# Performance work log

Measured on AMD Instinct MI355X. Metric: run time of the kernel, lower is better.

## Reference

```python
import jax, jax.numpy as jnp
import numpy as np

B, T, D, H, O = 128, 512, 128, 256, 1


def setup_inputs() -> dict:
    key = jax.random.key(0)
    ks = jax.random.split(key, 11)
    s = lambda n: 1.0 / np.sqrt(H)
    u = lambda k, shape: jax.random.uniform(k, shape, jnp.float32, -s(0), s(0))
    return {
        "X": jax.random.normal(ks[0], (B, T, D), jnp.float32),
        "Wih0": u(ks[1], (4 * H, D)),
        "Whh0": u(ks[2], (4 * H, H)),
        "bih0": u(ks[3], (4 * H,)),
        "bhh0": u(ks[4], (4 * H,)),
        "Wih1": u(ks[5], (4 * H, H)),
        "Whh1": u(ks[6], (4 * H, H)),
        "bih1": u(ks[7], (4 * H,)),
        "bhh1": u(ks[8], (4 * H,)),
        "Wfc": u(ks[9], (O, H)),
        "bfc": u(ks[10], (O,)),
    }


def _lstm_layer(x, Wih, Whh, bih, bhh):
    # x: [B, T, Din] -> h sequence [B, T, H]
    # Precompute input contributions for all timesteps (one big GEMM).
    xg = jnp.einsum("btd,gd->btg", x, Wih) + bih + bhh  # [B, T, 4H]
    xg = jnp.transpose(xg, (1, 0, 2))  # [T, B, 4H]
    h0 = jnp.zeros((x.shape[0], Whh.shape[1]), x.dtype)
    c0 = jnp.zeros_like(h0)

    def step(carry, xt):
        h, c = carry
        gates = xt + h @ Whh.T  # [B, 4H]
        i, f, g, o = jnp.split(gates, 4, axis=-1)  # PyTorch gate order i,f,g,o
        i = jax.nn.sigmoid(i)
        f = jax.nn.sigmoid(f)
        g = jnp.tanh(g)
        o = jax.nn.sigmoid(o)
        c = f * c + i * g
        h = o * jnp.tanh(c)
        return (h, c), h

    (_, _), hs = jax.lax.scan(step, (h0, c0), xg)
    return jnp.transpose(hs, (1, 0, 2))  # [B, T, H]


def reference(X, Wih0, Whh0, bih0, bhh0, Wih1, Whh1, bih1, bhh1, Wfc, bfc):
    h1 = _lstm_layer(X, Wih0, Whh0, bih0, bhh0)
    h2 = _lstm_layer(h1, Wih1, Whh1, bih1, bhh1)
    return h2[:, -1, :] @ Wfc.T + bfc  # [B, O]
```

## Files before the change

kernel.cpp:

```cpp
#include <hip/hip_runtime.h>

typedef unsigned short u16;
typedef unsigned int u32;
typedef __attribute__((ext_vector_type(8))) short bf8;
typedef __attribute__((ext_vector_type(4))) float f4;

#define DEVI static __device__ __forceinline__

constexpr int Bb = 128, Tt = 512, Dd = 128, Hh = 256, G4 = 1024;
constexpr int CH  = 32;
constexpr int NCH = Tt / CH;
constexpr int MCH = CH * Bb;
constexpr size_t CHF = (size_t)MCH * G4;

DEVI u16 f2bf(float f) {
  union { float f; u32 u; } v; v.f = f;
  u32 r = v.u + 0x7FFFu + ((v.u >> 16) & 1u);
  return (u16)(r >> 16);
}
DEVI float bf2f(u16 b) { union { u32 u; float f; } v; v.u = ((u32)b) << 16; return v.f; }
DEVI float frcp(float x) { return __builtin_amdgcn_rcpf(x); }
DEVI float sigm(float x) { return frcp(1.f + __expf(-x)); }
DEVI float tanh_f(float x) { return 1.f - 2.f * frcp(1.f + __expf(2.f * x)); }
DEVI f4 mfma16(bf8 a, bf8 b, f4 c) {
  return __builtin_amdgcn_mfma_f32_16x16x32_bf16(a, b, c, 0, 0, 0);
}

DEVI u32 ld_u32_coh(const u32* p) {
  u32 r;
  asm volatile("global_load_dword %0, %1, off sc0 sc1\ns_waitcnt vmcnt(0)"
               : "=&v"(r) : "v"(p) : "memory");
  return r;
}
DEVI bf8 ld16_coh(const u16* p) {
  bf8 r;
  asm volatile("global_load_dwordx4 %0, %1, off sc0 sc1" : "=&v"(r) : "v"(p) : "memory");
  return r;
}
DEVI void st16_coh(u16* p, bf8 v) {
  asm volatile("global_store_dwordx4 %0, %1, off sc0 sc1" :: "v"(p), "v"(v) : "memory");
}
DEVI void st_u32_coh(u32* p, u32 v) {
  asm volatile("global_store_dword %0, %1, off sc0 sc1" :: "v"(p), "v"(v) : "memory");
}
DEVI f4 ld16f(const float* p) {
  f4 r;
  asm volatile("global_load_dwordx4 %0, %1, off" : "=&v"(r) : "v"(p) : "memory");
  return r;
}


__global__ void k_prep_x(const float* __restrict__ X, u16* __restrict__ Xhi, u16* __restrict__ Xlo) {
  size_t idx = (size_t)blockIdx.x * 256 + threadIdx.x;
  int d = (int)(idx % Dd);
  size_t bt = idx / Dd;
  int b = (int)(bt / Tt), t = (int)(bt % Tt);
  float x = X[idx];
  u16 hi = f2bf(x);
  u16 lo = f2bf(x - bf2f(hi));
  size_t o = ((size_t)t * Bb + b) * Dd + d;
  Xhi[o] = hi; Xlo[o] = lo;
}

__global__ void k_split(const float* __restrict__ W, u16* __restrict__ hi_, u16* __restrict__ lo_) {
  size_t idx = (size_t)blockIdx.x * 256 + threadIdx.x;
  float v = W[idx];
  u16 hi = f2bf(v);
  hi_[idx] = hi;
  lo_[idx] = f2bf(v - bf2f(hi));
}

__global__ void k_prep_whh(const float* __restrict__ Whh, u16* __restrict__ W2) {
  int idx = blockIdx.x * 256 + threadIdx.x;
  int i = idx & 7, lane = (idx >> 3) & 63, kt = (idx >> 9) & 7, jtg = idx >> 12;
  int jp = (jtg << 4) + (lane & 15);
  int k  = ((lane >> 4) << 3) + i + (kt << 5);
  W2[idx] = f2bf(Whh[(size_t)jp * Hh + k]);
}

__global__ void k_bias(const float* __restrict__ a, const float* __restrict__ b, float* __restrict__ o) {
  int i = blockIdx.x * 256 + threadIdx.x;
  if (i < G4) o[i] = a[i] + b[i];
}

__global__ void k_init(u32* __restrict__ tags) {
  int i = blockIdx.x * 256 + threadIdx.x;
  if (i < 2 * (Tt + 1) * 64) {
    int row = (i >> 6) % (Tt + 1);
    tags[i] = (row == 0) ? 1u : 0u;
  }
}

__global__ void k_zrow(u16* __restrict__ a, u16* __restrict__ b) {
  int i = blockIdx.x * 256 + threadIdx.x;
  if (i < Bb * Hh) { a[i] = 0; b[i] = 0; }
}

template <int K, bool ALO>
DEVI void gemm_body(char* smem, const u16* __restrict__ Ahi, const u16* __restrict__ Alo,
                    const u16* __restrict__ Whi, const u16* __restrict__ Wlo,
                    const float* __restrict__ bias, float* __restrict__ Cout,
                    int bx, int by) {
  u16* AsH = (u16*)smem;
  u16* AsL = (u16*)(smem + 8192);
  const int tid = threadIdx.x, l = tid & 63;
  const int w = tid >> 6, wm = w >> 1, wn = w & 1;
  const int lrow = l & 15, lk = (l >> 4) << 3;
  const size_t m0 = (size_t)bx * 128;
  const int n0 = by * 128;

  f4 acc[4][4];
  size_t colK[4];
#pragma unroll
  for (int ni = 0; ni < 4; ++ni) {
    int col = n0 + wn * 64 + ni * 16 + lrow;
    float bv = bias[col];
    colK[ni] = (size_t)col * K + lk;
#pragma unroll
    for (int mi = 0; mi < 4; ++mi) {
      acc[mi][ni][0] = bv; acc[mi][ni][1] = bv; acc[mi][ni][2] = bv; acc[mi][ni][3] = bv;
    }
  }

  for (int kk = 0; kk < K; kk += 32) {
    __syncthreads();
#pragma unroll
    for (int s = 0; s < 2; ++s) {
      int slot = s * 256 + tid;
      int r = slot >> 2, kg = (slot & 3) << 3;
      *(bf8*)&AsH[r * 32 + kg] = *(const bf8*)&Ahi[(m0 + r) * K + kk + kg];
      if constexpr (ALO) *(bf8*)&AsL[r * 32 + kg] = *(const bf8*)&Alo[(m0 + r) * K + kk + kg];
    }
    __syncthreads();

    bf8 bh[4], bl[4];
#pragma unroll
    for (int ni = 0; ni < 4; ++ni) {
      bh[ni] = *(const bf8*)&Whi[colK[ni] + kk];
      bl[ni] = *(const bf8*)&Wlo[colK[ni] + kk];
    }
    bf8 ah[4], al[4];
#pragma unroll
    for (int mi = 0; mi < 4; ++mi) {
      ah[mi] = *(const bf8*)&AsH[(wm * 64 + mi * 16 + lrow) * 32 + lk];
      if constexpr (ALO) al[mi] = *(const bf8*)&AsL[(wm * 64 + mi * 16 + lrow) * 32 + lk];
    }
#pragma unroll
    for (int mi = 0; mi < 4; ++mi)
#pragma unroll
      for (int ni = 0; ni < 4; ++ni) {
        acc[mi][ni] = mfma16(ah[mi], bh[ni], acc[mi][ni]);
        acc[mi][ni] = mfma16(ah[mi], bl[ni], acc[mi][ni]);
        if constexpr (ALO) acc[mi][ni] = mfma16(al[mi], bh[ni], acc[mi][ni]);
      }
  }

  f4* C4 = (f4*)Cout;
#pragma unroll
  for (int mi = 0; mi < 4; ++mi) {
    int gg = wm * 4 + mi;
#pragma unroll
    for (int ni = 0; ni < 4; ++ni) {
      int colb = by * 128 + wn * 64 + ni * 16;
      int q  = colb >> 8;
      int ss = (colb >> 5) & 7;
      int wt = (colb >> 4) & 1;
      C4[(((((size_t)bx * 8 + gg) * 8 + ss) * 2 + wt) * 4 + q) * 64 + l] = acc[mi][ni];
    }
  }
}

DEVI void recur_body(char* smem, const float* __restrict__ xg, const u16* __restrict__ W2,
                     u16* h, float* cst, u32* tags,
                     int t0, int role, int sub) {
  u16* wlds = (u16*)smem;
  u16* sbuf = (u16*)(smem + 65536);
  const int tid = threadIdx.x, l = tid & 63, w = tid >> 6;
  const int lrow = l & 15, lg = l >> 4;
  const int g = sub & 7, s = sub >> 3;
  const int b_base = g << 4;
  const int w1 = w & 1;

  for (int u = 0; u < 16; ++u) {
    int f = u * 256 + tid;
    int jl = f >> 9, kt = (f >> 6) & 7, e = f & 63;
    int jtg = ((jl >> 1) << 4) + (s << 1) + (jl & 1);
    *(bf8*)&wlds[f << 3] = *(const bf8*)&W2[((size_t)jtg << 12) + (kt << 9) + (e << 3)];
  }

  const int jmy = (s << 5) + (w1 << 4) + lrow;
  float cc4[4] = {0.f, 0.f, 0.f, 0.f};
  if (tid < 128 && t0 > 0) {
#pragma unroll
    for (int rr = 0; rr < 4; ++rr)
      cc4[rr] = cst[(size_t)(b_base + (lg << 2) + rr) * Hh + jmy];
  }
  __syncthreads();

  const f4* xb = (const f4*)xg + ((((size_t)g * 8 + s) * 2 + w1) * 4) * 64 + l;
  f4 xgn[4];
  if (tid < 128) {
#pragma unroll
    for (int q = 0; q < 4; ++q) xgn[q] = ld16f((const float*)(xb + (q << 6)));
  }

  for (int t = 0; t <= CH; ++t) {
    const int T = t0 + t;

    if (tid < 128 && t < CH) {
      const u32 tagv = (u32)(T + 1);
      u32* tp = tags + ((((size_t)role * (Tt + 1) + T) * 8 + g) << 3) + (tid & 7);
      const u16* hr = h + ((size_t)(role ? (T & 1) : T) * Bb + b_base + lrow) * Hh + (lg << 3);

      int seen = (ld_u32_coh(tp) == tagv);
      bf8 af[8];
#pragma unroll
      for (int kt = 0; kt < 8; ++kt) af[kt] = ld16_coh(hr + (kt << 5));
      if (!__all(seen)) {
        int it = 0;
        do { seen = (ld_u32_coh(tp) == tagv); } while (!__all(seen) && ++it < (1 << 20));
#pragma unroll
        for (int kt = 0; kt < 8; ++kt) af[kt] = ld16_coh(hr + (kt << 5));
      }
      __builtin_amdgcn_sched_barrier(0);

      f4 acc[4];
#pragma unroll
      for (int q = 0; q < 4; ++q) acc[q] = xgn[q];

      bf8 bcur[4], bnxt[4];
#pragma unroll
      for (int q = 0; q < 4; ++q)
        bcur[q] = *(const bf8*)&wlds[((((q << 1) | w1) << 3) << 9) + (l << 3)];
#pragma unroll
      for (int kt = 0; kt < 8; ++kt) {
        if (kt < 7) {
#pragma unroll
          for (int q = 0; q < 4; ++q)
            bnxt[q] = *(const bf8*)&wlds[(((((q << 1) | w1) << 3) | (kt + 1)) << 9) + (l << 3)];
        }
        asm volatile("s_waitcnt vmcnt(%0)" :: "i"(7 - kt) : "memory");
        __builtin_amdgcn_sched_barrier(0);
#pragma unroll
        for (int q = 0; q < 4; ++q) acc[q] = mfma16(af[kt], bcur[q], acc[q]);
#pragma unroll
        for (int q = 0; q < 4; ++q) bcur[q] = bnxt[q];
      }

      if (t + 1 < CH) {
#pragma unroll
        for (int q = 0; q < 4; ++q)
          xgn[q] = ld16f((const float*)(xb + (size_t)(t + 1) * 32768 + (q << 6)));
      }

      u16 hv[4];
#pragma unroll
      for (int rr = 0; rr < 4; ++rr) {
        float gi = sigm(acc[0][rr]);
        float gf = sigm(acc[1][rr]);
        float gg = tanh_f(acc[2][rr]);
        float go = sigm(acc[3][rr]);
        float c2 = gf * cc4[rr] + gi * gg;
        cc4[rr] = c2;
        hv[rr] = f2bf(go * tanh_f(c2));
      }
#pragma unroll
      for (int rr = 0; rr < 4; ++rr)
        sbuf[((t & 1) << 9) + (((lg << 2) + rr) << 5) + (w1 << 4) + lrow] = hv[rr];
    } else if (tid >= 128 && tid < 192 && t > 0) {
      int u = tid - 128;
      int b = u >> 2, gg = u & 3;
      bf8 v = *(const bf8*)&sbuf[(((t - 1) & 1) << 9) + (b << 5) + (gg << 3)];
      u16* hw = h + ((size_t)(role ? (T & 1) : T) * Bb + b_base + b) * Hh
                + (s << 5) + (gg << 3);
      st16_coh(hw, v);
      asm volatile("s_waitcnt vmcnt(0)" ::: "memory");
      if (u == 0)
        st_u32_coh(tags + ((((size_t)role * (Tt + 1) + T) * 8 + g) << 3) + s, (u32)(T + 1));
    }
    asm volatile("s_waitcnt lgkmcnt(0)\ns_barrier" ::: "memory");
  }

  if (tid < 128) {
#pragma unroll
    for (int rr = 0; rr < 4; ++rr)
      cst[(size_t)(b_base + (lg << 2) + rr) * Hh + jmy] = cc4[rr];
  }
}

__global__ void __launch_bounds__(256) k_mega(
    const u16* gAh, const u16* gAl,
    const u16* W0h, const u16* W0l, const float* b0,
    const u16* gBa,
    const u16* W1h, const u16* W1l, const float* b1,
    float* xgAw, const float* xgAr,
    float* xgBw, const float* xgBr,
    const u16* W2a, const u16* W2b,
    u16* h1, u16* h2r, float* cstA, float* cstB,
    u32* tags, int d) {
  __shared__ __align__(16) char smem[67584];
  const int bid = blockIdx.x;
  if (bid < 128) {
    const int role = bid >> 6;
    if (role == 0) {
      if (d < 1 || d > NCH) return;
      recur_body(smem, xgAr, W2a, h1, cstA, tags, (d - 1) * CH, 0, bid & 63);
    } else {
      if (d < 3 || d > NCH + 2) return;
      recur_body(smem, xgBr, W2b, h2r, cstB, tags, (d - 3) * CH, 1, bid & 63);
    }
  } else if (bid < 384) {
    if (d > NCH - 1) return;
    int q = bid - 128;
    gemm_body<Dd, true>(smem, gAh, gAl, W0h, W0l, b0, xgAw, q & 31, q >> 5);
  } else {
    if (d < 2 || d > NCH + 1) return;
    int q = bid - 384;
    gemm_body<Hh, false>(smem, gBa, nullptr, W1h, W1l, b1, xgBw, q & 31, q >> 5);
  }
}

__global__ void k_fc(const u16* __restrict__ h2l, const float* __restrict__ Wfc,
                     const float* __restrict__ bfc, float* __restrict__ out) {
  int b = threadIdx.x;
  if (b < Bb) {
    float s = bfc[0];
    for (int j = 0; j < Hh; ++j) s += bf2f(h2l[(size_t)b * Hh + j]) * Wfc[j];
    out[b] = s;
  }
}

extern "C" void kernel_launch(void* const* d_in, const int* in_sizes, int n_in,
                              void* d_out, int out_size, void* d_ws, size_t ws_size,
                              hipStream_t stream) {
  const float* X    = (const float*)d_in[0];
  const float* Wih0 = (const float*)d_in[1];
  const float* Whh0 = (const float*)d_in[2];
  const float* bih0 = (const float*)d_in[3];
  const float* bhh0 = (const float*)d_in[4];
  const float* Wih1 = (const float*)d_in[5];
  const float* Whh1 = (const float*)d_in[6];
  const float* bih1 = (const float*)d_in[7];
  const float* bhh1 = (const float*)d_in[8];
  const float* Wfc  = (const float*)d_in[9];
  const float* bfc  = (const float*)d_in[10];

  char* base = (char*)d_ws;
  size_t off = 0;
  auto alloc = [&](size_t bytes) -> char* {
    char* p = base + off;
    off = (off + bytes + 255) & ~(size_t)255;
    return p;
  };

  u16* Xhi = (u16*)alloc((size_t)Bb * Tt * Dd * 2);
  u16* Xlo = (u16*)alloc((size_t)Bb * Tt * Dd * 2);
  u16* W0h = (u16*)alloc((size_t)G4 * Dd * 2);
  u16* W0l = (u16*)alloc((size_t)G4 * Dd * 2);
  u16* W1h = (u16*)alloc((size_t)G4 * Hh * 2);
  u16* W1l = (u16*)alloc((size_t)G4 * Hh * 2);
  u16* W2a = (u16*)alloc((size_t)G4 * Hh * 2);
  u16* W2b = (u16*)alloc((size_t)G4 * Hh * 2);
  float* b0 = (float*)alloc(G4 * 4);
  float* b1 = (float*)alloc(G4 * 4);
  float* xgA = (float*)alloc((size_t)2 * CHF * 4);
  float* xgB = (float*)alloc((size_t)2 * CHF * 4);
  u16* h1Z = (u16*)alloc((size_t)(Tt + 1) * Bb * Hh * 2);
  u16* h2r = (u16*)alloc((size_t)2 * Bb * Hh * 2);
  float* cstA = (float*)alloc((size_t)Bb * Hh * 4);
  float* cstB = (float*)alloc((size_t)Bb * Hh * 4);
  u32* tags = (u32*)alloc((size_t)2 * (Tt + 1) * 64 * 4);

  k_init<<<(2 * (Tt + 1) * 64 + 255) / 256, 256, 0, stream>>>(tags);
  k_zrow<<<(Bb * Hh + 255) / 256, 256, 0, stream>>>(h1Z, h2r);
  k_prep_x<<<(Bb * Tt * Dd) / 256, 256, 0, stream>>>(X, Xhi, Xlo);
  k_split<<<(G4 * Dd) / 256, 256, 0, stream>>>(Wih0, W0h, W0l);
  k_split<<<(G4 * Hh) / 256, 256, 0, stream>>>(Wih1, W1h, W1l);
  k_prep_whh<<<(G4 * Hh) / 256, 256, 0, stream>>>(Whh0, W2a);
  k_prep_whh<<<(G4 * Hh) / 256, 256, 0, stream>>>(Whh1, W2b);
  k_bias<<<4, 256, 0, stream>>>(bih0, bhh0, b0);
  k_bias<<<4, 256, 0, stream>>>(bih1, bhh1, b1);

  for (int dd = 0; dd <= NCH + 2; ++dd) {
    int ca = dd < NCH ? dd : NCH - 1;
    int cb = dd < 2 ? 0 : (dd - 2 < NCH ? dd - 2 : NCH - 1);
    k_mega<<<640, 256, 0, stream>>>(
        Xhi + (size_t)ca * MCH * Dd, Xlo + (size_t)ca * MCH * Dd,
        W0h, W0l, b0,
        h1Z + (size_t)(cb * CH + 1) * Bb * Hh,
        W1h, W1l, b1,
        xgA + (size_t)(dd & 1) * CHF, xgA + (size_t)((dd + 1) & 1) * CHF,
        xgB + (size_t)(dd & 1) * CHF, xgB + (size_t)((dd + 1) & 1) * CHF,
        W2a, W2b, h1Z, h2r, cstA, cstB, tags, dd);
  }
  k_fc<<<1, 128, 0, stream>>>(h2r, Wfc, bfc, (float*)d_out);

  (void)in_sizes; (void)n_in; (void)out_size; (void)ws_size;
}
```

Baseline: 1.803 ms.

## Let compute waves publish hidden state directly, dropping LDS staging and barrier

The recurrent block no longer stages each step's h through shared memory to a separate writer wave with a per-step block barrier. Each of the two compute waves now writes its own bf16 h values with coherent short stores and raises its own flag, so the tag table doubles to 16 flags per group. This removes one step of latency per timestep on the serial critical path and drops the per-step barrier. In exchange it issues many scattered 2-byte stores instead of 16-byte vector stores, and consumers now poll twice as many flags.

```diff
diff --git a/kernel.cpp b/kernel.cpp
--- a/kernel.cpp
+++ b/kernel.cpp
@@ -37,8 +37,8 @@
   asm volatile("global_load_dwordx4 %0, %1, off sc0 sc1" : "=&v"(r) : "v"(p) : "memory");
   return r;
 }
-DEVI void st16_coh(u16* p, bf8 v) {
-  asm volatile("global_store_dwordx4 %0, %1, off sc0 sc1" :: "v"(p), "v"(v) : "memory");
+DEVI void st2_coh(u16* p, u32 v) {
+  asm volatile("global_store_short %0, %1, off sc0 sc1" :: "v"(p), "v"(v) : "memory");
 }
 DEVI void st_u32_coh(u32* p, u32 v) {
   asm volatile("global_store_dword %0, %1, off sc0 sc1" :: "v"(p), "v"(v) : "memory");
@@ -85,8 +85,8 @@
 
 __global__ void k_init(u32* __restrict__ tags) {
   int i = blockIdx.x * 256 + threadIdx.x;
-  if (i < 2 * (Tt + 1) * 64) {
-    int row = (i >> 6) % (Tt + 1);
+  if (i < 2 * (Tt + 1) * 128) {
+    int row = (i >> 7) % (Tt + 1);
     tags[i] = (row == 0) ? 1u : 0u;
   }
 }
@@ -174,12 +174,10 @@
                      u16* h, float* cst, u32* tags,
                      int t0, int role, int sub) {
   u16* wlds = (u16*)smem;
-  u16* sbuf = (u16*)(smem + 65536);
   const int tid = threadIdx.x, l = tid & 63, w = tid >> 6;
   const int lrow = l & 15, lg = l >> 4;
   const int g = sub & 7, s = sub >> 3;
   const int b_base = g << 4;
-  const int w1 = w & 1;
 
   for (int u = 0; u < 16; ++u) {
     int f = u * 256 + tid;
@@ -187,105 +185,95 @@
     int jtg = ((jl >> 1) << 4) + (s << 1) + (jl & 1);
     *(bf8*)&wlds[f << 3] = *(const bf8*)&W2[((size_t)jtg << 12) + (kt << 9) + (e << 3)];
   }
-
+  __syncthreads();
+  if (w >= 2) return;
+
+  const int w1 = w;
   const int jmy = (s << 5) + (w1 << 4) + lrow;
   float cc4[4] = {0.f, 0.f, 0.f, 0.f};
-  if (tid < 128 && t0 > 0) {
+  if (t0 > 0) {
 #pragma unroll
     for (int rr = 0; rr < 4; ++rr)
       cc4[rr] = cst[(size_t)(b_base + (lg << 2) + rr) * Hh + jmy];
   }
-  __syncthreads();
 
   const f4* xb = (const f4*)xg + ((((size_t)g * 8 + s) * 2 + w1) * 4) * 64 + l;
   f4 xgn[4];
-  if (tid < 128) {
-#pragma unroll
-    for (int q = 0; q < 4; ++q) xgn[q] = ld16f((const float*)(xb + (q << 6)));
-  }
-
-  for (int t = 0; t <= CH; ++t) {
+#pragma unroll
+  for (int q = 0; q < 4; ++q) xgn[q] = ld16f((const float*)(xb + (q << 6)));
+
+  for (int t = 0; t < CH; ++t) {
     const int T = t0 + t;
-
-    if (tid < 128 && t < CH) {
-      const u32 tagv = (u32)(T + 1);
-      u32* tp = tags + ((((size_t)role * (Tt + 1) + T) * 8 + g) << 3) + (tid & 7);
-      const u16* hr = h + ((size_t)(role ? (T & 1) : T) * Bb + b_base + lrow) * Hh + (lg << 3);
-
-      int seen = (ld_u32_coh(tp) == tagv);
-      bf8 af[8];
+    const u32 tagv = (u32)(T + 1);
+    u32* tp = tags + ((((size_t)role * (Tt + 1) + T) * 8 + g) << 4) + (l & 15);
+    const u16* hr = h + ((size_t)(role ? (T & 1) : T) * Bb + b_base + lrow) * Hh + (lg << 3);
+
+    int seen = (ld_u32_coh(tp) == tagv);
+    bf8 af[8];
+#pragma unroll
+    for (int kt = 0; kt < 8; ++kt) af[kt] = ld16_coh(hr + (kt << 5));
+    if (!__all(seen)) {
+      int it = 0;
+      do { seen = (ld_u32_coh(tp) == tagv); } while (!__all(seen) && ++it < (1 << 20));
 #pragma unroll
       for (int kt = 0; kt < 8; ++kt) af[kt] = ld16_coh(hr + (kt << 5));
-      if (!__all(seen)) {
-        int it = 0;
-        do { seen = (ld_u32_coh(tp) == tagv); } while (!__all(seen) && ++it < (1 << 20));
-#pragma unroll
-        for (int kt = 0; kt < 8; ++kt) af[kt] = ld16_coh(hr + (kt << 5));
+    }
+    __builtin_amdgcn_sched_barrier(0);
+
+    f4 acc[4];
+#pragma unroll
+    for (int q = 0; q < 4; ++q) acc[q] = xgn[q];
+
+    bf8 bcur[4], bnxt[4];
+#pragma unroll
+    for (int q = 0; q < 4; ++q)
+      bcur[q] = *(const bf8*)&wlds[((((q << 1) | w1) << 3) << 9) + (l << 3)];
+#pragma unroll
+    for (int kt = 0; kt < 8; ++kt) {
+      if (kt < 7) {
+#pragma unroll
+        for (int q = 0; q < 4; ++q)
+          bnxt[q] = *(const bf8*)&wlds[(((((q << 1) | w1) << 3) | (kt + 1)) << 9) + (l << 3)];
       }
+      asm volatile("s_waitcnt vmcnt(%0)" :: "i"(7 - kt) : "memory");
       __builtin_amdgcn_sched_barrier(0);
-
-      f4 acc[4];
-#pragma unroll
-      for (int q = 0; q < 4; ++q) acc[q] = xgn[q];
-
-      bf8 bcur[4], bnxt[4];
+#pragma unroll
+      for (int q = 0; q < 4; ++q) acc[q] = mfma16(af[kt], bcur[q], acc[q]);
+#pragma unroll
+      for (int q = 0; q < 4; ++q) bcur[q] = bnxt[q];
+    }
+
+    if (t + 1 < CH) {
 #pragma unroll
       for (int q = 0; q < 4; ++q)
-        bcur[q] = *(const bf8*)&wlds[((((q << 1) | w1) << 3) << 9) + (l << 3)];
-#pragma unroll
-      for (int kt = 0; kt < 8; ++kt) {
-        if (kt < 7) {
-#pragma unroll
-          for (int q = 0; q < 4; ++q)
-            bnxt[q] = *(const bf8*)&wlds[(((((q << 1) | w1) << 3) | (kt + 1)) << 9) + (l << 3)];
-        }
-        asm volatile("s_waitcnt vmcnt(%0)" :: "i"(7 - kt) : "memory");
-        __builtin_amdgcn_sched_barrier(0);
-#pragma unroll
-        for (int q = 0; q < 4; ++q) acc[q] = mfma16(af[kt], bcur[q], acc[q]);
-#pragma unroll
-        for (int q = 0; q < 4; ++q) bcur[q] = bnxt[q];
-      }
-
-      if (t + 1 < CH) {
-#pragma unroll
-        for (int q = 0; q < 4; ++q)
-          xgn[q] = ld16f((const float*)(xb + (size_t)(t + 1) * 32768 + (q << 6)));
-      }
-
-      u16 hv[4];
-#pragma unroll
-      for (int rr = 0; rr < 4; ++rr) {
-        float gi = sigm(acc[0][rr]);
-        float gf = sigm(acc[1][rr]);
-        float gg = tanh_f(acc[2][rr]);
-        float go = sigm(acc[3][rr]);
-        float c2 = gf * cc4[rr] + gi * gg;
-        cc4[rr] = c2;
-        hv[rr] = f2bf(go * tanh_f(c2));
-      }
-#pragma unroll
-      for (int rr = 0; rr < 4; ++rr)
-        sbuf[((t & 1) << 9) + (((lg << 2) + rr) << 5) + (w1 << 4) + lrow] = hv[rr];
-    } else if (tid >= 128 && tid < 192 && t > 0) {
-      int u = tid - 128;
-      int b = u >> 2, gg = u & 3;
-      bf8 v = *(const bf8*)&sbuf[(((t - 1) & 1) << 9) + (b << 5) + (gg << 3)];
-      u16* hw = h + ((size_t)(role ? (T & 1) : T) * Bb + b_base + b) * Hh
-                + (s << 5) + (gg << 3);
-      st16_coh(hw, v);
-      asm volatile("s_waitcnt vmcnt(0)" ::: "memory");
-      if (u == 0)
-        st_u32_coh(tags + ((((size_t)role * (Tt + 1) + T) * 8 + g) << 3) + s, (u32)(T + 1));
-    }
-    asm volatile("s_waitcnt lgkmcnt(0)\ns_barrier" ::: "memory");
-  }
-
-  if (tid < 128) {
+        xgn[q] = ld16f((const float*)(xb + (size_t)(t + 1) * 32768 + (q << 6)));
+    }
+
+    u16 hv[4];
+#pragma unroll
+    for (int rr = 0; rr < 4; ++rr) {
+      float gi = sigm(acc[0][rr]);
+      float gf = sigm(acc[1][rr]);
+      float gg = tanh_f(acc[2][rr]);
+      float go = sigm(acc[3][rr]);
+      float c2 = gf * cc4[rr] + gi * gg;
+      cc4[rr] = c2;
+      hv[rr] = f2bf(go * tanh_f(c2));
+    }
+
+    u16* hw = h + ((size_t)(role ? ((T + 1) & 1) : (T + 1)) * Bb + b_base) * Hh + jmy;
 #pragma unroll
     for (int rr = 0; rr < 4; ++rr)
-      cst[(size_t)(b_base + (lg << 2) + rr) * Hh + jmy] = cc4[rr];
-  }
+      st2_coh(hw + (size_t)((lg << 2) + rr) * Hh, (u32)hv[rr]);
+    asm volatile("s_waitcnt vmcnt(0)" ::: "memory");
+    if (l == 0)
+      st_u32_coh(tags + ((((size_t)role * (Tt + 1) + T + 1) * 8 + g) << 4) + (s << 1) + w1,
+                 (u32)(T + 2));
+  }
+
+#pragma unroll
+  for (int rr = 0; rr < 4; ++rr)
+    cst[(size_t)(b_base + (lg << 2) + rr) * Hh + jmy] = cc4[rr];
 }
 
 __global__ void __launch_bounds__(256) k_mega(
@@ -298,7 +286,7 @@
     const u16* W2a, const u16* W2b,
     u16* h1, u16* h2r, float* cstA, float* cstB,
     u32* tags, int d) {
-  __shared__ __align__(16) char smem[67584];
+  __shared__ __align__(16) char smem[66560];
   const int bid = blockIdx.x;
   if (bid < 128) {
     const int role = bid >> 6;
@@ -369,9 +357,9 @@
   u16* h2r = (u16*)alloc((size_t)2 * Bb * Hh * 2);
   float* cstA = (float*)alloc((size_t)Bb * Hh * 4);
   float* cstB = (float*)alloc((size_t)Bb * Hh * 4);
-  u32* tags = (u32*)alloc((size_t)2 * (Tt + 1) * 64 * 4);
-
-  k_init<<<(2 * (Tt + 1) * 64 + 255) / 256, 256, 0, stream>>>(tags);
+  u32* tags = (u32*)alloc((size_t)2 * (Tt + 1) * 128 * 4);
+
+  k_init<<<(2 * (Tt + 1) * 128 + 255) / 256, 256, 0, stream>>>(tags);
   k_zrow<<<(Bb * Hh + 255) / 256, 256, 0, stream>>>(h1Z, h2r);
   k_prep_x<<<(Bb * Tt * Dd) / 256, 256, 0, stream>>>(X, Xhi, Xlo);
   k_split<<<(G4 * Dd) / 256, 256, 0, stream>>>(Wih0, W0h, W0l);
```

Result: faster. 1.742 ms (-3.4%).
